# Kernel optimization log

Measured on AMD Instinct MI355X. Metric: run time of the kernel, lower is better.

## Reference

```python
import jax, jax.numpy as jnp
import numpy as np

D_MODEL = 768
KERNELS = [7, 5, 3]
FILTERS = [40, 30, 20]
FC_IN = sum(FILTERS)  # 90


def setup_inputs() -> dict:
    key = jax.random.key(0)
    ks = jax.random.split(key, 16)
    B, S, D = 8, 2048, D_MODEL
    inp = {
        'x1': jax.random.normal(ks[0], (B, S, D), jnp.float32),
        'x2': jax.random.normal(ks[1], (B, S, D), jnp.float32),
    }
    # conv weights: OIH layout [out_ch, in_ch, k]
    for i, (k, f) in enumerate(zip(KERNELS, FILTERS)):
        scale = 1.0 / np.sqrt(D * k)
        inp[f'w{k}'] = jax.random.uniform(ks[2 + 2 * i], (f, D, k), jnp.float32, -scale, scale)
        inp[f'b{k}'] = jax.random.uniform(ks[3 + 2 * i], (f,), jnp.float32, -scale, scale)
    inp['U'] = jax.random.normal(ks[8], (D, D), jnp.float32) * (1.0 / np.sqrt(D))
    inp['bias_v'] = jax.random.normal(ks[9], (D,), jnp.float32) * 0.02
    inp['fc_w'] = jax.random.normal(ks[10], (D, FC_IN), jnp.float32) * (1.0 / np.sqrt(FC_IN))
    inp['fc_b'] = jnp.zeros((D,), jnp.float32)
    inp['fcx_w'] = jax.random.normal(ks[11], (D, 2 * D), jnp.float32) * (1.0 / np.sqrt(2 * D))
    inp['fcx_b'] = jnp.zeros((D,), jnp.float32)
    return inp


def _conv1d_same(x_ncs, w_oik, b_o, k):
    # x: [B, C, S], w: [O, C, k] -> [B, O, S], 'same' padding = k//2
    y = jax.lax.conv_general_dilated(
        x_ncs, w_oik, window_strides=(1,), padding=[(k // 2, k // 2)],
        dimension_numbers=('NCH', 'OIH', 'NCH'))
    return y + b_o[None, :, None]


def reference(x1, x2, w7, b7, w5, b5, w3, b3, U, bias_v, fc_w, fc_b, fcx_w, fcx_b):
    # CNN branch over x2 (dropout layers are identity in eval mode)
    xc = jnp.transpose(x2, (0, 2, 1))  # [B, D, S]
    feats = jnp.concatenate([
        jnp.transpose(_conv1d_same(xc, w7, b7, 7), (0, 2, 1)),
        jnp.transpose(_conv1d_same(xc, w5, b5, 5), (0, 2, 1)),
        jnp.transpose(_conv1d_same(xc, w3, b3, 3), (0, 2, 1)),
    ], axis=-1)                                    # [B, S, 90]
    x = jnp.tanh(jax.nn.relu(feats) @ fc_w.T + fc_b)  # [B, S, D]
    # biaffine attention: x1 @ U @ x2^T + x2 @ bias (broadcast over rows)
    attn = jnp.einsum('bsd,de,bte->bst', x1, U, x2) + (x2 @ bias_v)[:, None, :]
    attn = jax.nn.softmax(attn, axis=-1)           # [B, S, S]
    out = jnp.tanh(attn @ x2)                      # [B, S, D]
    x = x + out
    return jnp.concatenate([x1, x], axis=-1) @ fcx_w.T + fcx_b  # [B, S, D]
```

## Files before the change

### kernel.cpp

```cpp
#include <hip/hip_runtime.h>
#include <cmath>

#define D_MODEL 768
#define SEQ 2048
#define BATCH 8
#define FC_PAD 96
#define FC_PAD2 128
#define KCOMB (7 * D_MODEL)
#define KCHUNK 2688

typedef unsigned short ushort_t;
typedef _Float16 half_t;
typedef __attribute__((ext_vector_type(8))) _Float16 f16x8;
typedef __attribute__((ext_vector_type(8))) unsigned short u16x8;
typedef __attribute__((ext_vector_type(4))) unsigned short u16x4;
typedef __attribute__((ext_vector_type(4))) float f32x4;

struct Ptr8 { const ushort_t* p[8]; };

__device__ __forceinline__ ushort_t f2h(float x) {
    half_t h = (half_t)x;
    return __builtin_bit_cast(ushort_t, h);
}
__device__ __forceinline__ float h2f(ushort_t u) {
    return (float)__builtin_bit_cast(half_t, u);
}
__device__ __forceinline__ float fast_tanh(float x) {
    float a = fabsf(x);
    float t = __expf(-2.f * a);
    float r = (1.f - t) / (1.f + t);
    return copysignf(r, x);
}
__device__ __forceinline__ void gload16(const ushort_t* g, ushort_t* lbase) {
    __builtin_amdgcn_global_load_lds((const __attribute__((address_space(1))) void*)g,
                                     (__attribute__((address_space(3))) void*)lbase,
                                     16, 0, 0);
}

__global__ void convert_f16_kernel(const float* __restrict__ src, ushort_t* __restrict__ dst, size_t n4) {
    size_t i = (size_t)blockIdx.x * 256 + threadIdx.x;
    if (i >= n4) return;
    f32x4 x = *(const f32x4*)(src + i * 4);
    u16x4 h;
    #pragma unroll
    for (int j = 0; j < 4; ++j) h[j] = f2h(x[j]);
    *(u16x4*)(dst + i * 4) = h;
}

__global__ void convert_fc_kernel(const float* __restrict__ src, ushort_t* __restrict__ dst) {
    int i = blockIdx.x * 256 + threadIdx.x;
    if (i >= D_MODEL * FC_PAD2) return;
    int o = i / FC_PAD2, j = i - o * FC_PAD2;
    dst[i] = (j < 90) ? f2h(src[o * 90 + j]) : 0;
}

__global__ void convert_ut_kernel(const float* __restrict__ U, ushort_t* __restrict__ dst) {
    int i = blockIdx.x * 256 + threadIdx.x;
    if (i >= D_MODEL * D_MODEL) return;
    int n = i / D_MODEL, k = i - n * D_MODEL;
    dst[i] = f2h(U[(size_t)k * D_MODEL + n]);
}

__global__ void build_wcomb_kernel(const float* __restrict__ w7, const float* __restrict__ b7,
                                   const float* __restrict__ w5, const float* __restrict__ b5,
                                   const float* __restrict__ w3, const float* __restrict__ b3,
                                   ushort_t* __restrict__ Wt, float* __restrict__ bcat) {
    int idx = blockIdx.x * 256 + threadIdx.x;
    const int total = FC_PAD2 * KCOMB;
    if (idx < total) {
        int o = idx / KCOMB, k = idx - o * KCOMB;
        int t = k / D_MODEL, d = k - t * D_MODEL;
        float v = 0.f;
        if (o < 40) {
            v = w7[(size_t)o * (D_MODEL * 7) + d * 7 + t];
        } else if (o < 70) {
            int t5 = t - 1;
            if (t5 >= 0 && t5 < 5) v = w5[(size_t)(o - 40) * (D_MODEL * 5) + d * 5 + t5];
        } else if (o < 90) {
            int t3 = t - 2;
            if (t3 >= 0 && t3 < 3) v = w3[(size_t)(o - 70) * (D_MODEL * 3) + d * 3 + t3];
        }
        Wt[idx] = f2h(v);
    }
    if (idx < FC_PAD2) {
        float bv = 0.f;
        if (idx < 40) bv = b7[idx];
        else if (idx < 70) bv = b5[idx - 40];
        else if (idx < 90) bv = b3[idx - 70];
        bcat[idx] = bv;
    }
}

__global__ void conv_reduce_kernel(const float* __restrict__ P, const float* __restrict__ bcat,
                                   ushort_t* __restrict__ feats) {
    const size_t MT = (size_t)BATCH * SEQ;
    size_t i = (size_t)blockIdx.x * 256 + threadIdx.x;
    if (i >= MT * FC_PAD2) return;
    int col = (int)(i & (FC_PAD2 - 1));
    size_t row = i >> 7;
    float v = 0.f;
    if (col < FC_PAD) {
        size_t idx = row * FC_PAD + col;
        const size_t st = MT * FC_PAD;
        v = P[idx] + P[idx + st] + bcat[col];
        v = fmaxf(v, 0.f);
    }
    feats[i] = f2h(v);
}

__global__ void transpose_f16_kernel(const ushort_t* __restrict__ in, ushort_t* __restrict__ out) {
    __shared__ ushort_t tile[32][40];
    int b = blockIdx.z;
    int s0 = blockIdx.x * 32, d0 = blockIdx.y * 32;
    int tx = threadIdx.x & 31, ty = threadIdx.x >> 5;
    const ushort_t* inb = in + (size_t)b * SEQ * D_MODEL;
    ushort_t* outb = out + (size_t)b * D_MODEL * SEQ;
    #pragma unroll
    for (int i = 0; i < 4; ++i)
        tile[ty + i * 8][tx] = inb[(size_t)(s0 + ty + i * 8) * D_MODEL + d0 + tx];
    __syncthreads();
    #pragma unroll
    for (int i = 0; i < 4; ++i)
        outb[(size_t)(d0 + ty + i * 8) * SEQ + s0 + tx] = tile[tx][ty + i * 8];
}

template<int TM, int TN, int AMODE, int ACT, int HASBIAS, int HASADD,
         int OUTMODE, int KSPLIT, int APTR, int MAP, int ZM, int GX, int GY,
         int SMEPI, int ASCALE>
__global__ __launch_bounds__(256, 3)
void mfma_gemm(const ushort_t* __restrict__ A, const ushort_t* __restrict__ A2,
               const ushort_t* __restrict__ B, const float* __restrict__ bias,
               const ushort_t* __restrict__ addsrc,
               float* __restrict__ Cf, ushort_t* __restrict__ Ch,
               Ptr8 ap, float* __restrict__ smw, float* __restrict__ slw,
               int M, int N, int K, int lda, int ldb, int ldc,
               size_t sA, size_t sB, size_t sBias, size_t sC) {
    constexpr int WM = TM / 2, WN = TN / 2, FM = WM / 16, FN = WN / 16;
    __shared__ __align__(16) ushort_t As_[TM * 64];
    __shared__ __align__(16) ushort_t Bs_[TN * 64];
    __shared__ float pmS[SMEPI ? 4 : 1][SMEPI ? 64 : 1];
    __shared__ float msS[SMEPI ? 128 : 1];
    __shared__ float plS[SMEPI ? 4 : 1][SMEPI ? 64 : 1];
    __shared__ ushort_t alS[ASCALE ? 16 : 1][ASCALE ? 128 : 1];

    int bx, by, z;
    if (MAP == 1) {
        int lin = blockIdx.x;
        z = lin % ZM;
        int t = lin / ZM;
        bx = t % GX;
        by = t / GX;
    } else if (MAP == 2) {
        int lin = blockIdx.x;
        int xcd = lin & 7;
        int t = lin >> 3;
        by = t % GY;
        bx = xcd * (GX / 8) + t / GY;
        z = 0;
    } else if (MAP == 3) {
        int lin = blockIdx.x;
        z = lin % ZM;
        int t = lin / ZM;
        by = t % GY;
        bx = t / GY;
    } else {
        bx = blockIdx.x; by = blockIdx.y; z = blockIdx.z;
    }

    const int kb = KSPLIT ? z * K : 0;
    const ushort_t* Ab = APTR ? ap.p[z] : (A + (KSPLIT ? 0 : (size_t)z * sA));
    const ushort_t* Bb = B + (KSPLIT ? 0 : (size_t)z * sB);
    if (HASBIAS) bias += (size_t)z * sBias;
    if (HASADD) addsrc += (size_t)z * sC;
    if (OUTMODE == 0) Cf += (size_t)z * sC;
    else if (!SMEPI) Ch += (size_t)z * sC;

    const int m0 = bx * TM;
    const int n0 = by * TN;
    const int tid = threadIdx.x;
    const int lane = tid & 63;
    const int wave = tid >> 6;
    const int wm = (wave >> 1) * WM, wn = (wave & 1) * WN;
    const int r16 = lane & 15, kq = lane >> 4;
    const int srow = tid >> 3;
    const int slot = tid & 7;

    if (ASCALE) {
        if (tid < 128) {
            int row = tid;
            int gm = m0 + row;
            float mt[16], al[16];
            float mg = -3.0e38f;
            #pragma unroll
            for (int t = 0; t < 16; ++t) {
                mt[t] = smw[((size_t)z * 16 + t) * SEQ + gm];
                mg = fmaxf(mg, mt[t]);
            }
            float lg = 0.f;
            #pragma unroll
            for (int t = 0; t < 16; ++t) {
                float e = __expf(mt[t] - mg);
                lg += slw[((size_t)z * 16 + t) * SEQ + gm] * e;
                al[t] = e;
            }
            float inv = 1.f / lg;
            #pragma unroll
            for (int t = 0; t < 16; ++t) alS[t][row] = f2h(al[t] * inv);
        }
        __syncthreads();
    }

    f32x4 acc[FM][FN];
    #pragma unroll
    for (int i = 0; i < FM; ++i)
        #pragma unroll
        for (int j = 0; j < FN; ++j) acc[i][j] = (f32x4){0.f, 0.f, 0.f, 0.f};

    const u16x8 zv = {0, 0, 0, 0, 0, 0, 0, 0};

    for (int k0 = 0; k0 < K; k0 += 64) {
        #pragma unroll
        for (int i = 0; i < TM / 32; ++i) {
            int row = i * 32 + srow;
            int gm = m0 + row;
            int xs = slot ^ (row & 7);
            if (AMODE == 1) {
                int gkk = kb + k0 + xs * 8;
                int t = gkk / D_MODEL, d = gkk - t * D_MODEL;
                int s = (gm & (SEQ - 1)) + t - 3;
                int bb = gm >> 11;
                u16x8 v = (s >= 0 && s < SEQ) ? *(const u16x8*)(Ab + ((size_t)(bb * SEQ + s)) * lda + d) : zv;
                *(u16x8*)&As_[(size_t)row * 64 + slot * 8] = v;
            } else {
                const ushort_t* src;
                if (AMODE == 2) {
                    int gk = k0 + xs * 8;
                    src = (gk < D_MODEL) ? Ab + (size_t)gm * D_MODEL + gk
                                         : A2 + (size_t)gm * D_MODEL + (gk - D_MODEL);
                } else {
                    int gk = kb + k0 + xs * 8;
                    src = Ab + (size_t)gm * lda + gk;
                }
                gload16(src, &As_[(size_t)(i * 32 + wave * 8) * 64]);
            }
        }
        #pragma unroll
        for (int i = 0; i < TN / 32; ++i) {
            int row = i * 32 + srow;
            int gn = n0 + row;
            int xs = slot ^ (row & 7);
            int gk = kb + k0 + xs * 8;
            gload16(Bb + (size_t)gn * ldb + gk, &Bs_[(size_t)(i * 32 + wave * 8) * 64]);
        }
        __syncthreads();

        f16x8 ah[FM][2], bh[FN][2];
        #pragma unroll
        for (int mi = 0; mi < FM; ++mi) {
            int row = wm + mi * 16 + r16;
            #pragma unroll
            for (int kk = 0; kk < 2; ++kk)
                ah[mi][kk] = *(const f16x8*)&As_[(size_t)row * 64 + (((kk * 4 + kq) ^ (row & 7)) * 8)];
        }
        if (ASCALE) {
            const int kt = k0 >> 7;
            #pragma unroll
            for (int mi = 0; mi < FM; ++mi) {
                half_t s = __builtin_bit_cast(half_t, alS[kt][wm + mi * 16 + r16]);
                ah[mi][0] = ah[mi][0] * s;
                ah[mi][1] = ah[mi][1] * s;
            }
        }
        #pragma unroll
        for (int ni = 0; ni < FN; ++ni) {
            int row = wn + ni * 16 + r16;
            #pragma unroll
            for (int kk = 0; kk < 2; ++kk)
                bh[ni][kk] = *(const f16x8*)&Bs_[(size_t)row * 64 + (((kk * 4 + kq) ^ (row & 7)) * 8)];
        }
        #pragma unroll
        for (int kk = 0; kk < 2; ++kk)
            #pragma unroll
            for (int mi = 0; mi < FM; ++mi)
                #pragma unroll
                for (int ni = 0; ni < FN; ++ni)
                    acc[mi][ni] = __builtin_amdgcn_mfma_f32_16x16x32_f16(ah[mi][kk], bh[ni][kk], acc[mi][ni], 0, 0, 0);
        __syncthreads();
    }

    if (SMEPI) {
        float pmax[FM][4];
        #pragma unroll
        for (int mi = 0; mi < FM; ++mi)
            #pragma unroll
            for (int r = 0; r < 4; ++r) {
                float mx = -3.0e38f;
                #pragma unroll
                for (int ni = 0; ni < FN; ++ni) {
                    float v = acc[mi][ni][r];
                    if (HASBIAS) { v += bias[n0 + wn + ni * 16 + r16]; acc[mi][ni][r] = v; }
                    mx = fmaxf(mx, v);
                }
                mx = fmaxf(mx, __shfl_xor(mx, 1));
                mx = fmaxf(mx, __shfl_xor(mx, 2));
                mx = fmaxf(mx, __shfl_xor(mx, 4));
                mx = fmaxf(mx, __shfl_xor(mx, 8));
                pmax[mi][r] = mx;
            }
        if (r16 == 0) {
            #pragma unroll
            for (int mi = 0; mi < FM; ++mi)
                #pragma unroll
                for (int r = 0; r < 4; ++r)
                    pmS[wave][mi * 16 + kq * 4 + r] = pmax[mi][r];
        }
        __syncthreads();
        if (tid < 128) {
            int rl = tid & 63, grp = tid >> 6;
            msS[grp * 64 + rl] = fmaxf(pmS[grp * 2][rl], pmS[grp * 2 + 1][rl]);
        }
        __syncthreads();
        #pragma unroll
        for (int mi = 0; mi < FM; ++mi)
            #pragma unroll
            for (int r = 0; r < 4; ++r) {
                float mrow = msS[wm + mi * 16 + kq * 4 + r];
                float s = 0.f;
                #pragma unroll
                for (int ni = 0; ni < FN; ++ni) {
                    float e = __expf(acc[mi][ni][r] - mrow);
                    acc[mi][ni][r] = e;
                    s += e;
                }
                s += __shfl_xor(s, 1);
                s += __shfl_xor(s, 2);
                s += __shfl_xor(s, 4);
                s += __shfl_xor(s, 8);
                pmax[mi][r] = s;
            }
        if (r16 == 0) {
            #pragma unroll
            for (int mi = 0; mi < FM; ++mi)
                #pragma unroll
                for (int r = 0; r < 4; ++r)
                    plS[wave][mi * 16 + kq * 4 + r] = pmax[mi][r];
        }
        __syncthreads();
        if (tid < 128) {
            int rl = tid & 63, grp = tid >> 6;
            int row = grp * 64 + rl;
            float l2 = plS[grp * 2][rl] + plS[grp * 2 + 1][rl];
            size_t si = ((size_t)z * 16 + by) * SEQ + (m0 + row);
            smw[si] = msS[row];
            slw[si] = l2;
        }
        ushort_t* Co = (ushort_t*)ap.p[z];
        #pragma unroll
        for (int mi = 0; mi < FM; ++mi)
            #pragma unroll
            for (int ni = 0; ni < FN; ++ni)
                #pragma unroll
                for (int r = 0; r < 4; ++r) {
                    int gm = m0 + wm + mi * 16 + kq * 4 + r;
                    int gn = n0 + wn + ni * 16 + r16;
                    Co[(size_t)gm * SEQ + gn] = f2h(acc[mi][ni][r]);
                }
        return;
    }

    #pragma unroll
    for (int mi = 0; mi < FM; ++mi)
        #pragma unroll
        for (int ni = 0; ni < FN; ++ni)
            #pragma unroll
            for (int r = 0; r < 4; ++r) {
                int gm = m0 + wm + mi * 16 + kq * 4 + r;
                int gn = n0 + wn + ni * 16 + r16;
                if (gn >= N) continue;
                float v = acc[mi][ni][r];
                if (HASBIAS) v += bias[gn];
                if (ACT == 1) v = fmaxf(v, 0.f);
                else if (ACT == 2) v = fast_tanh(v);
                if (HASADD) v += h2f(addsrc[(size_t)gm * ldc + gn]);
                size_t idx = (size_t)gm * ldc + gn;
                if (OUTMODE == 0) Cf[idx] = v;
                else Ch[idx] = f2h(v);
            }
}

extern "C" void kernel_launch(void* const* d_in, const int* in_sizes, int n_in,
                              void* d_out, int out_size, void* d_ws, size_t ws_size,
                              hipStream_t stream) {
    const float* x1     = (const float*)d_in[0];
    const float* x2     = (const float*)d_in[1];
    const float* w7     = (const float*)d_in[2];
    const float* b7     = (const float*)d_in[3];
    const float* w5     = (const float*)d_in[4];
    const float* b5     = (const float*)d_in[5];
    const float* w3     = (const float*)d_in[6];
    const float* b3     = (const float*)d_in[7];
    const float* U      = (const float*)d_in[8];
    const float* bias_v = (const float*)d_in[9];
    const float* fc_w   = (const float*)d_in[10];
    const float* fc_b   = (const float*)d_in[11];
    const float* fcx_w  = (const float*)d_in[12];
    const float* fcx_b  = (const float*)d_in[13];
    float* out = (float*)d_out;

    const size_t MT = (size_t)BATCH * SEQ;
    const size_t NE = MT * D_MODEL;
    const size_t NEb = (size_t)SEQ * D_MODEL;
    const size_t SEGSZ = (size_t)SEQ * SEQ;

    char* p = (char*)d_ws;
    auto alloc = [&](size_t bytes) -> char* {
        char* r = p;
        p += (bytes + 255) & ~(size_t)255;
        return r;
    };
    ushort_t* x1_h   = (ushort_t*)alloc(NE * 2);
    ushort_t* x2_h   = (ushort_t*)alloc(NE * 2);
    ushort_t* x2t    = (ushort_t*)alloc(NE * 2);
    ushort_t* y1     = (ushort_t*)alloc(NE * 2);
    ushort_t* xcnn   = (ushort_t*)alloc(NE * 2);
    float*    convp  = (float*)   alloc(MT * FC_PAD * 4 * 4);
    ushort_t* feats  = (ushort_t*)alloc(MT * FC_PAD2 * 2);
    ushort_t* Wt     = (ushort_t*)alloc((size_t)FC_PAD2 * KCOMB * 2);
    ushort_t* fc_wt  = (ushort_t*)alloc((size_t)D_MODEL * FC_PAD2 * 2);
    ushort_t* fcx_wt = (ushort_t*)alloc((size_t)D_MODEL * 2 * D_MODEL * 2);
    ushort_t* Ut     = (ushort_t*)alloc((size_t)D_MODEL * D_MODEL * 2);
    float*    bcat   = (float*)alloc(FC_PAD2 * 4);
    float*    smS    = (float*)alloc((size_t)BATCH * 16 * SEQ * 4);
    float*    slS    = (float*)alloc((size_t)BATCH * 16 * SEQ * 4);

    ushort_t* dob = (ushort_t*)d_out;
    Ptr8 ap;
    ap.p[0] = (ushort_t*)convp;
    ap.p[1] = (ushort_t*)convp + SEGSZ;
    ap.p[2] = (ushort_t*)convp + 2 * SEGSZ;
    ap.p[3] = dob;
    ap.p[4] = dob + SEGSZ;
    ap.p[5] = dob + 2 * SEGSZ;
    ap.p[6] = dob + 3 * SEGSZ;
    ap.p[7] = dob + 4 * SEGSZ;
    Ptr8 apz = {};

    const int T = 256;
    auto blk = [](size_t n) { return dim3((unsigned)((n + 255) / 256)); };

    build_wcomb_kernel<<<blk((size_t)FC_PAD2 * KCOMB), T, 0, stream>>>(w7, b7, w5, b5, w3, b3, Wt, bcat);
    convert_fc_kernel<<<blk((size_t)D_MODEL * FC_PAD2), T, 0, stream>>>(fc_w, fc_wt);
    convert_f16_kernel<<<blk((size_t)D_MODEL * 2 * D_MODEL / 4), T, 0, stream>>>(fcx_w, fcx_wt, (size_t)D_MODEL * 2 * D_MODEL / 4);
    convert_ut_kernel<<<blk((size_t)D_MODEL * D_MODEL), T, 0, stream>>>(U, Ut);
    convert_f16_kernel<<<blk(NE / 4), T, 0, stream>>>(x1, x1_h, NE / 4);
    convert_f16_kernel<<<blk(NE / 4), T, 0, stream>>>(x2, x2_h, NE / 4);
    transpose_f16_kernel<<<dim3(SEQ / 32, D_MODEL / 32, BATCH), T, 0, stream>>>(x2_h, x2t);

    mfma_gemm<64, 128, 1, 0, 0, 0, 0, 1, 0, 0, 1, 1, 1, 0, 0><<<dim3(MT / 64, 1, 2), T, 0, stream>>>(
        x2_h, nullptr, Wt, nullptr, nullptr,
        convp, nullptr, apz, nullptr, nullptr,
        (int)MT, FC_PAD, KCHUNK, D_MODEL, KCOMB, FC_PAD,
        0, 0, 0, MT * FC_PAD);
    conv_reduce_kernel<<<blk(MT * FC_PAD2), T, 0, stream>>>(convp, bcat, feats);

    mfma_gemm<128, 128, 0, 2, 1, 0, 1, 0, 0, 2, 1, 128, 6, 0, 0><<<dim3(768, 1, 1), T, 0, stream>>>(
        feats, nullptr, fc_wt, fc_b, nullptr,
        nullptr, xcnn, apz, nullptr, nullptr,
        (int)MT, D_MODEL, FC_PAD2, FC_PAD2, FC_PAD2, D_MODEL, 0, 0, 0, 0);

    mfma_gemm<128, 128, 0, 0, 1, 0, 1, 0, 0, 2, 1, 128, 6, 0, 0><<<dim3(768, 1, 1), T, 0, stream>>>(
        x1_h, nullptr, Ut, bias_v, nullptr,
        nullptr, y1, apz, nullptr, nullptr,
        (int)MT, D_MODEL, D_MODEL, D_MODEL, D_MODEL, D_MODEL, 0, 0, 0, 0);

    mfma_gemm<128, 128, 0, 0, 0, 0, 1, 0, 0, 1, 8, 16, 16, 1, 0><<<dim3(2048, 1, 1), T, 0, stream>>>(
        y1, nullptr, x2_h, nullptr, nullptr,
        nullptr, nullptr, ap, smS, slS,
        SEQ, SEQ, D_MODEL, D_MODEL, D_MODEL, SEQ,
        NEb, NEb, 0, 0);

    mfma_gemm<128, 128, 0, 2, 0, 1, 1, 0, 1, 3, 8, 16, 6, 0, 1><<<dim3(768, 1, 1), T, 0, stream>>>(
        nullptr, nullptr, x2t, nullptr,
        xcnn,
        nullptr, xcnn, ap, smS, slS,
        SEQ, D_MODEL, SEQ, SEQ, SEQ, D_MODEL,
        0, NEb, 0, NEb);

    mfma_gemm<128, 128, 2, 0, 1, 0, 0, 0, 0, 2, 1, 128, 6, 0, 0><<<dim3(768, 1, 1), T, 0, stream>>>(
        x1_h, xcnn, fcx_wt, fcx_b, nullptr,
        out, nullptr, apz, nullptr, nullptr,
        (int)MT, D_MODEL, 2 * D_MODEL, D_MODEL, 2 * D_MODEL, D_MODEL, 0, 0, 0, 0);
}
```

Baseline: 340.0 us.

## Add dedicated 256x256 double-buffered scores kernel with fused softmax-stat epilogue

Replaces the generic 128x128 attention-score GEMM with a dedicated 512-thread kernel that uses 256x256 tiles, double-buffered LDS staging with explicit waitcnt and barriers, and MFMA priority raising. It keeps the per-tile row max and sum epilogue. The number of column tiles per row drops from 16 to 8, so the stats buffers and the ASCALE rescale in the PV GEMM are adjusted to match. The aim is more data reuse per loaded tile and overlap of global loads with MFMA work, at the cost of higher register and LDS pressure and fewer blocks. The generic GEMM also drops its SMEPI path and raises its occupancy hint from 3 to 4 blocks.

```diff
diff --git a/kernel.cpp b/kernel.cpp
--- a/kernel.cpp
+++ b/kernel.cpp
@@ -8,6 +8,7 @@
 #define FC_PAD2 128
 #define KCOMB (7 * D_MODEL)
 #define KCHUNK 2688
+#define NT_SC (D_MODEL / 64)
 
 typedef unsigned short ushort_t;
 typedef _Float16 half_t;
@@ -124,24 +125,178 @@
         outb[(size_t)(d0 + ty + i * 8) * SEQ + s0 + tx] = tile[tx][ty + i * 8];
 }
 
+__global__ __launch_bounds__(512, 2)
+void scores_kernel(const ushort_t* __restrict__ Abase, const ushort_t* __restrict__ Bbase,
+                   Ptr8 ap, float* __restrict__ smw, float* __restrict__ slw) {
+    __shared__ __align__(16) ushort_t As_[2][2][256][32];
+    __shared__ __align__(16) ushort_t Bs_[2][2][256][32];
+    __shared__ float pmW[4][256];
+    __shared__ float msS[256];
+    __shared__ float plW[4][256];
+
+    const int lin = blockIdx.x;
+    const int z = lin & 7;
+    const int t6 = lin >> 3;
+    const int bx = t6 & 7, by = t6 >> 3;
+    const ushort_t* A = Abase + (size_t)z * SEQ * D_MODEL;
+    const ushort_t* B = Bbase + (size_t)z * SEQ * D_MODEL;
+    const int m0 = bx * 256, n0 = by * 256;
+
+    const int tid = threadIdx.x;
+    const int lane = tid & 63;
+    const int wave = tid >> 6;
+    const int wm2 = wave >> 2;
+    const int wn4 = wave & 3;
+    const int r16 = lane & 15, kq = lane >> 4;
+    const int srow = tid >> 2;
+    const int sslot = tid & 3;
+
+    auto swz3 = [](int row) { return (row & 3) ^ ((row >> 2) & 1); };
+
+    auto STAGE = [&](int buf, int kh, int kbase) {
+        #pragma unroll
+        for (int i = 0; i < 2; ++i) {
+            int row = i * 128 + srow;
+            int gk = kbase + kh * 32 + ((sslot ^ swz3(row)) << 3);
+            gload16(A + (size_t)(m0 + row) * D_MODEL + gk, &As_[buf][kh][i * 128 + wave * 16][0]);
+        }
+        #pragma unroll
+        for (int i = 0; i < 2; ++i) {
+            int row = i * 128 + srow;
+            int gk = kbase + kh * 32 + ((sslot ^ swz3(row)) << 3);
+            gload16(B + (size_t)(n0 + row) * D_MODEL + gk, &Bs_[buf][kh][i * 128 + wave * 16][0]);
+        }
+    };
+
+    f32x4 acc[8][4];
+    #pragma unroll
+    for (int i = 0; i < 8; ++i)
+        #pragma unroll
+        for (int j = 0; j < 4; ++j) acc[i][j] = (f32x4){0.f, 0.f, 0.f, 0.f};
+
+    STAGE(0, 0, 0);
+    STAGE(0, 1, 0);
+    asm volatile("s_waitcnt vmcnt(0)" ::: "memory");
+    __builtin_amdgcn_sched_barrier(0);
+    __builtin_amdgcn_s_barrier();
+    __builtin_amdgcn_sched_barrier(0);
+
+    for (int t = 0; t < NT_SC; ++t) {
+        const int buf = t & 1;
+        const int kbn = (t + 1) * 64;
+        #pragma unroll
+        for (int kk = 0; kk < 2; ++kk) {
+            f16x8 af[8], bf[4];
+            #pragma unroll
+            for (int mi = 0; mi < 8; ++mi) {
+                int row = wm2 * 128 + mi * 16 + r16;
+                af[mi] = *(const f16x8*)&As_[buf][kk][row][(kq ^ swz3(row)) << 3];
+            }
+            #pragma unroll
+            for (int ni = 0; ni < 4; ++ni) {
+                int row = wn4 * 64 + ni * 16 + r16;
+                bf[ni] = *(const f16x8*)&Bs_[buf][kk][row][(kq ^ swz3(row)) << 3];
+            }
+            if (t + 1 < NT_SC) STAGE(buf ^ 1, kk, kbn);
+            asm volatile("s_waitcnt vmcnt(4)" ::: "memory");
+            asm volatile("s_waitcnt lgkmcnt(0)" ::: "memory");
+            __builtin_amdgcn_sched_barrier(0);
+            __builtin_amdgcn_s_setprio(1);
+            #pragma unroll
+            for (int mi = 0; mi < 8; ++mi)
+                #pragma unroll
+                for (int ni = 0; ni < 4; ++ni)
+                    acc[mi][ni] = __builtin_amdgcn_mfma_f32_16x16x32_f16(af[mi], bf[ni], acc[mi][ni], 0, 0, 0);
+            __builtin_amdgcn_s_setprio(0);
+            __builtin_amdgcn_sched_barrier(0);
+            __builtin_amdgcn_s_barrier();
+            __builtin_amdgcn_sched_barrier(0);
+        }
+    }
+
+    float red[8][4];
+    #pragma unroll
+    for (int mi = 0; mi < 8; ++mi)
+        #pragma unroll
+        for (int r = 0; r < 4; ++r) {
+            float mx = fmaxf(fmaxf(acc[mi][0][r], acc[mi][1][r]), fmaxf(acc[mi][2][r], acc[mi][3][r]));
+            mx = fmaxf(mx, __shfl_xor(mx, 1));
+            mx = fmaxf(mx, __shfl_xor(mx, 2));
+            mx = fmaxf(mx, __shfl_xor(mx, 4));
+            mx = fmaxf(mx, __shfl_xor(mx, 8));
+            red[mi][r] = mx;
+        }
+    if (r16 == 0) {
+        #pragma unroll
+        for (int mi = 0; mi < 8; ++mi)
+            #pragma unroll
+            for (int r = 0; r < 4; ++r)
+                pmW[wn4][wm2 * 128 + mi * 16 + kq * 4 + r] = red[mi][r];
+    }
+    __syncthreads();
+    if (tid < 256)
+        msS[tid] = fmaxf(fmaxf(pmW[0][tid], pmW[1][tid]), fmaxf(pmW[2][tid], pmW[3][tid]));
+    __syncthreads();
+    #pragma unroll
+    for (int mi = 0; mi < 8; ++mi)
+        #pragma unroll
+        for (int r = 0; r < 4; ++r) {
+            float m = msS[wm2 * 128 + mi * 16 + kq * 4 + r];
+            float s = 0.f;
+            #pragma unroll
+            for (int ni = 0; ni < 4; ++ni) {
+                float e = __expf(acc[mi][ni][r] - m);
+                acc[mi][ni][r] = e;
+                s += e;
+            }
+            s += __shfl_xor(s, 1);
+            s += __shfl_xor(s, 2);
+            s += __shfl_xor(s, 4);
+            s += __shfl_xor(s, 8);
+            red[mi][r] = s;
+        }
+    if (r16 == 0) {
+        #pragma unroll
+        for (int mi = 0; mi < 8; ++mi)
+            #pragma unroll
+            for (int r = 0; r < 4; ++r)
+                plW[wn4][wm2 * 128 + mi * 16 + kq * 4 + r] = red[mi][r];
+    }
+    __syncthreads();
+    if (tid < 256) {
+        float l = plW[0][tid] + plW[1][tid] + plW[2][tid] + plW[3][tid];
+        size_t si = ((size_t)z * 8 + by) * SEQ + (m0 + tid);
+        smw[si] = msS[tid];
+        slw[si] = l;
+    }
+    ushort_t* Co = (ushort_t*)ap.p[z];
+    #pragma unroll
+    for (int mi = 0; mi < 8; ++mi)
+        #pragma unroll
+        for (int ni = 0; ni < 4; ++ni)
+            #pragma unroll
+            for (int r = 0; r < 4; ++r) {
+                int gm = m0 + wm2 * 128 + mi * 16 + kq * 4 + r;
+                int gn = n0 + wn4 * 64 + ni * 16 + r16;
+                Co[(size_t)gm * SEQ + gn] = f2h(acc[mi][ni][r]);
+            }
+}
+
 template<int TM, int TN, int AMODE, int ACT, int HASBIAS, int HASADD,
          int OUTMODE, int KSPLIT, int APTR, int MAP, int ZM, int GX, int GY,
-         int SMEPI, int ASCALE>
-__global__ __launch_bounds__(256, 3)
+         int ASCALE>
+__global__ __launch_bounds__(256, 4)
 void mfma_gemm(const ushort_t* __restrict__ A, const ushort_t* __restrict__ A2,
                const ushort_t* __restrict__ B, const float* __restrict__ bias,
                const ushort_t* __restrict__ addsrc,
                float* __restrict__ Cf, ushort_t* __restrict__ Ch,
-               Ptr8 ap, float* __restrict__ smw, float* __restrict__ slw,
+               Ptr8 ap, const float* __restrict__ smw, const float* __restrict__ slw,
                int M, int N, int K, int lda, int ldb, int ldc,
                size_t sA, size_t sB, size_t sBias, size_t sC) {
     constexpr int WM = TM / 2, WN = TN / 2, FM = WM / 16, FN = WN / 16;
     __shared__ __align__(16) ushort_t As_[TM * 64];
     __shared__ __align__(16) ushort_t Bs_[TN * 64];
-    __shared__ float pmS[SMEPI ? 4 : 1][SMEPI ? 64 : 1];
-    __shared__ float msS[SMEPI ? 128 : 1];
-    __shared__ float plS[SMEPI ? 4 : 1][SMEPI ? 64 : 1];
-    __shared__ ushort_t alS[ASCALE ? 16 : 1][ASCALE ? 128 : 1];
+    __shared__ ushort_t alS[ASCALE ? 8 : 1][ASCALE ? 128 : 1];
 
     int bx, by, z;
     if (MAP == 1) {
@@ -173,7 +328,7 @@
     if (HASBIAS) bias += (size_t)z * sBias;
     if (HASADD) addsrc += (size_t)z * sC;
     if (OUTMODE == 0) Cf += (size_t)z * sC;
-    else if (!SMEPI) Ch += (size_t)z * sC;
+    else Ch += (size_t)z * sC;
 
     const int m0 = bx * TM;
     const int n0 = by * TN;
@@ -189,23 +344,23 @@
         if (tid < 128) {
             int row = tid;
             int gm = m0 + row;
-            float mt[16], al[16];
+            float mt[8], al[8];
             float mg = -3.0e38f;
             #pragma unroll
-            for (int t = 0; t < 16; ++t) {
-                mt[t] = smw[((size_t)z * 16 + t) * SEQ + gm];
+            for (int t = 0; t < 8; ++t) {
+                mt[t] = smw[((size_t)z * 8 + t) * SEQ + gm];
                 mg = fmaxf(mg, mt[t]);
             }
             float lg = 0.f;
             #pragma unroll
-            for (int t = 0; t < 16; ++t) {
+            for (int t = 0; t < 8; ++t) {
                 float e = __expf(mt[t] - mg);
-                lg += slw[((size_t)z * 16 + t) * SEQ + gm] * e;
+                lg += slw[((size_t)z * 8 + t) * SEQ + gm] * e;
                 al[t] = e;
             }
             float inv = 1.f / lg;
             #pragma unroll
-            for (int t = 0; t < 16; ++t) alS[t][row] = f2h(al[t] * inv);
+            for (int t = 0; t < 8; ++t) alS[t][row] = f2h(al[t] * inv);
         }
         __syncthreads();
     }
@@ -263,7 +418,7 @@
                 ah[mi][kk] = *(const f16x8*)&As_[(size_t)row * 64 + (((kk * 4 + kq) ^ (row & 7)) * 8)];
         }
         if (ASCALE) {
-            const int kt = k0 >> 7;
+            const int kt = k0 >> 8;
             #pragma unroll
             for (int mi = 0; mi < FM; ++mi) {
                 half_t s = __builtin_bit_cast(half_t, alS[kt][wm + mi * 16 + r16]);
@@ -286,86 +441,6 @@
                 for (int ni = 0; ni < FN; ++ni)
                     acc[mi][ni] = __builtin_amdgcn_mfma_f32_16x16x32_f16(ah[mi][kk], bh[ni][kk], acc[mi][ni], 0, 0, 0);
         __syncthreads();
-    }
-
-    if (SMEPI) {
-        float pmax[FM][4];
-        #pragma unroll
-        for (int mi = 0; mi < FM; ++mi)
-            #pragma unroll
-            for (int r = 0; r < 4; ++r) {
-                float mx = -3.0e38f;
-                #pragma unroll
-                for (int ni = 0; ni < FN; ++ni) {
-                    float v = acc[mi][ni][r];
-                    if (HASBIAS) { v += bias[n0 + wn + ni * 16 + r16]; acc[mi][ni][r] = v; }
-                    mx = fmaxf(mx, v);
-                }
-                mx = fmaxf(mx, __shfl_xor(mx, 1));
-                mx = fmaxf(mx, __shfl_xor(mx, 2));
-                mx = fmaxf(mx, __shfl_xor(mx, 4));
-                mx = fmaxf(mx, __shfl_xor(mx, 8));
-                pmax[mi][r] = mx;
-            }
-        if (r16 == 0) {
-            #pragma unroll
-            for (int mi = 0; mi < FM; ++mi)
-                #pragma unroll
-                for (int r = 0; r < 4; ++r)
-                    pmS[wave][mi * 16 + kq * 4 + r] = pmax[mi][r];
-        }
-        __syncthreads();
-        if (tid < 128) {
-            int rl = tid & 63, grp = tid >> 6;
-            msS[grp * 64 + rl] = fmaxf(pmS[grp * 2][rl], pmS[grp * 2 + 1][rl]);
-        }
-        __syncthreads();
-        #pragma unroll
-        for (int mi = 0; mi < FM; ++mi)
-            #pragma unroll
-            for (int r = 0; r < 4; ++r) {
-                float mrow = msS[wm + mi * 16 + kq * 4 + r];
-                float s = 0.f;
-                #pragma unroll
-                for (int ni = 0; ni < FN; ++ni) {
-                    float e = __expf(acc[mi][ni][r] - mrow);
-                    acc[mi][ni][r] = e;
-                    s += e;
-                }
-                s += __shfl_xor(s, 1);
-                s += __shfl_xor(s, 2);
-                s += __shfl_xor(s, 4);
-                s += __shfl_xor(s, 8);
-                pmax[mi][r] = s;
-            }
-        if (r16 == 0) {
-            #pragma unroll
-            for (int mi = 0; mi < FM; ++mi)
-                #pragma unroll
-                for (int r = 0; r < 4; ++r)
-                    plS[wave][mi * 16 + kq * 4 + r] = pmax[mi][r];
-        }
-        __syncthreads();
-        if (tid < 128) {
-            int rl = tid & 63, grp = tid >> 6;
-            int row = grp * 64 + rl;
-            float l2 = plS[grp * 2][rl] + plS[grp * 2 + 1][rl];
-            size_t si = ((size_t)z * 16 + by) * SEQ + (m0 + row);
-            smw[si] = msS[row];
-            slw[si] = l2;
-        }
-        ushort_t* Co = (ushort_t*)ap.p[z];
-        #pragma unroll
-        for (int mi = 0; mi < FM; ++mi)
-            #pragma unroll
-            for (int ni = 0; ni < FN; ++ni)
-                #pragma unroll
-                for (int r = 0; r < 4; ++r) {
-                    int gm = m0 + wm + mi * 16 + kq * 4 + r;
-                    int gn = n0 + wn + ni * 16 + r16;
-                    Co[(size_t)gm * SEQ + gn] = f2h(acc[mi][ni][r]);
-                }
-        return;
     }
 
     #pragma unroll
@@ -430,8 +505,8 @@
     ushort_t* fcx_wt = (ushort_t*)alloc((size_t)D_MODEL * 2 * D_MODEL * 2);
     ushort_t* Ut     = (ushort_t*)alloc((size_t)D_MODEL * D_MODEL * 2);
     float*    bcat   = (float*)alloc(FC_PAD2 * 4);
-    float*    smS    = (float*)alloc((size_t)BATCH * 16 * SEQ * 4);
-    float*    slS    = (float*)alloc((size_t)BATCH * 16 * SEQ * 4);
+    float*    smS    = (float*)alloc((size_t)BATCH * 8 * SEQ * 4);
+    float*    slS    = (float*)alloc((size_t)BATCH * 8 * SEQ * 4);
 
     ushort_t* dob = (ushort_t*)d_out;
     Ptr8 ap;
@@ -456,37 +531,33 @@
     convert_f16_kernel<<<blk(NE / 4), T, 0, stream>>>(x2, x2_h, NE / 4);
     transpose_f16_kernel<<<dim3(SEQ / 32, D_MODEL / 32, BATCH), T, 0, stream>>>(x2_h, x2t);
 
-    mfma_gemm<64, 128, 1, 0, 0, 0, 0, 1, 0, 0, 1, 1, 1, 0, 0><<<dim3(MT / 64, 1, 2), T, 0, stream>>>(
+    mfma_gemm<64, 128, 1, 0, 0, 0, 0, 1, 0, 0, 1, 1, 1, 0><<<dim3(MT / 64, 1, 2), T, 0, stream>>>(
         x2_h, nullptr, Wt, nullptr, nullptr,
         convp, nullptr, apz, nullptr, nullptr,
         (int)MT, FC_PAD, KCHUNK, D_MODEL, KCOMB, FC_PAD,
         0, 0, 0, MT * FC_PAD);
     conv_reduce_kernel<<<blk(MT * FC_PAD2), T, 0, stream>>>(convp, bcat, feats);
 
-    mfma_gemm<128, 128, 0, 2, 1, 0, 1, 0, 0, 2, 1, 128, 6, 0, 0><<<dim3(768, 1, 1), T, 0, stream>>>(
+    mfma_gemm<128, 128, 0, 2, 1, 0, 1, 0, 0, 2, 1, 128, 6, 0><<<dim3(768, 1, 1), T, 0, stream>>>(
         feats, nullptr, fc_wt, fc_b, nullptr,
         nullptr, xcnn, apz, nullptr, nullptr,
         (int)MT, D_MODEL, FC_PAD2, FC_PAD2, FC_PAD2, D_MODEL, 0, 0, 0, 0);
 
-    mfma_gemm<128, 128, 0, 0, 1, 0, 1, 0, 0, 2, 1, 128, 6, 0, 0><<<dim3(768, 1, 1), T, 0, stream>>>(
+    mfma_gemm<128, 128, 0, 0, 1, 0, 1, 0, 0, 2, 1, 128, 6, 0><<<dim3(768, 1, 1), T, 0, stream>>>(
         x1_h, nullptr, Ut, bias_v, nullptr,
         nullptr, y1, apz, nullptr, nullptr,
         (int)MT, D_MODEL, D_MODEL, D_MODEL, D_MODEL, D_MODEL, 0, 0, 0, 0);
 
-    mfma_gemm<128, 128, 0, 0, 0, 0, 1, 0, 0, 1, 8, 16, 16, 1, 0><<<dim3(2048, 1, 1), T, 0, stream>>>(
-        y1, nullptr, x2_h, nullptr, nullptr,
-        nullptr, nullptr, ap, smS, slS,
-        SEQ, SEQ, D_MODEL, D_MODEL, D_MODEL, SEQ,
-        NEb, NEb, 0, 0);
-
-    mfma_gemm<128, 128, 0, 2, 0, 1, 1, 0, 1, 3, 8, 16, 6, 0, 1><<<dim3(768, 1, 1), T, 0, stream>>>(
+    scores_kernel<<<dim3(512, 1, 1), dim3(512), 0, stream>>>(y1, x2_h, ap, smS, slS);
+
+    mfma_gemm<128, 128, 0, 2, 0, 1, 1, 0, 1, 3, 8, 16, 6, 1><<<dim3(768, 1, 1), T, 0, stream>>>(
         nullptr, nullptr, x2t, nullptr,
         xcnn,
         nullptr, xcnn, ap, smS, slS,
         SEQ, D_MODEL, SEQ, SEQ, SEQ, D_MODEL,
         0, NEb, 0, NEb);
 
-    mfma_gemm<128, 128, 2, 0, 1, 0, 0, 0, 0, 2, 1, 128, 6, 0, 0><<<dim3(768, 1, 1), T, 0, stream>>>(
+    mfma_gemm<128, 128, 2, 0, 1, 0, 0, 0, 0, 2, 1, 128, 6, 0><<<dim3(768, 1, 1), T, 0, stream>>>(
         x1_h, xcnn, fcx_wt, fcx_b, nullptr,
         out, nullptr, apz, nullptr, nullptr,
         (int)MT, D_MODEL, 2 * D_MODEL, D_MODEL, 2 * D_MODEL, D_MODEL, 0, 0, 0, 0);
```

After: 346.7 us. About the same (+2.0%).
